# Performance work log

Measured on AMD Instinct MI355X. Metric: run time of the kernel, lower is better.

The kernel has to match this reference:

```python
import jax, jax.numpy as jnp
import numpy as np

EPS = 1e-6

def _phi(x):
    # elu(x) + 1 feature map
    return jax.nn.elu(x) + 1.0

def setup_inputs() -> dict:
    key = jax.random.key(0)
    kq, kk, kv = jax.random.split(key, 3)
    N, L, S, H, D, M = 8, 4096, 4096, 8, 64, 64
    queries = jax.random.normal(kq, (N, L, H, D), dtype=jnp.float32)
    keys = jax.random.normal(kk, (N, S, H, D), dtype=jnp.float32)
    values = jax.random.normal(kv, (N, S, H, M), dtype=jnp.float32)
    key_mask = jnp.ones((N, S), dtype=jnp.float32)  # key_lengths.float_matrix
    return {"queries": queries, "keys": keys, "values": values, "key_mask": key_mask}

def reference(queries, keys, values, key_mask):
    Q = _phi(queries)                                   # [N,L,H,D]
    K = _phi(keys) * key_mask[:, :, None, None]         # [N,S,H,D]
    KV = jnp.einsum('nshd,nshm->nhmd', K, values)       # [N,H,M,D]
    Z = 1.0 / (jnp.einsum('nlhd,nhd->nlh', Q, K.sum(axis=1)) + EPS)  # [N,L,H]
    V = jnp.einsum('nlhd,nhmd,nlh->nlhm', Q, KV, Z)     # [N,L,H,M]
    return V
```

## Files before the change

kernel.cpp:

```cpp
#include <hip/hip_runtime.h>


#define SLEN 4096
#define LLEN 4096
#define NHTOT 64
#define HD   512
#define NSPLIT 4
#define EPSF 1e-6f

__device__ __forceinline__ float phi(float x) {
    return x > 0.0f ? x + 1.0f : __expf(x);
}

__device__ __forceinline__ void fma4(float4& a, float s, const float4& b) {
    a.x = fmaf(s, b.x, a.x);
    a.y = fmaf(s, b.y, a.y);
    a.z = fmaf(s, b.z, a.z);
    a.w = fmaf(s, b.w, a.w);
}

__global__ __launch_bounds__(256)
void la_phase1(const float* __restrict__ Kg, const float* __restrict__ Vg,
               const float* __restrict__ maskg,
               float* __restrict__ KVp, float* __restrict__ Ksump) {
    __shared__ float kb[4][4096];
    __shared__ float vb[4][4096];
    __shared__ float ksb[16 * 64];

    const int tid  = threadIdx.x;
    const int w    = tid >> 6;
    const int lane = tid & 63;
    const int nh   = blockIdx.y;
    const int n    = nh >> 3;
    const int h    = nh & 7;
    const int sp   = blockIdx.x;

    const int sr4 = lane >> 4;
    const int c4  = (lane & 15) * 4;
    const int d0  = (lane & 7) * 8;
    const int m0  = (lane >> 3) * 8;

    float* kw = kb[w];
    float* vw = vb[w];

    const size_t base = (size_t)n * SLEN * HD + (size_t)h * 64;
    const float* mrow = maskg + (size_t)n * SLEN;

    float4 acc[8][2];
    #pragma unroll
    for (int i = 0; i < 8; ++i) {
        acc[i][0] = make_float4(0.f, 0.f, 0.f, 0.f);
        acc[i][1] = make_float4(0.f, 0.f, 0.f, 0.f);
    }
    float4 ksp = make_float4(0.f, 0.f, 0.f, 0.f);

    for (int t = 0; t < 4; ++t) {
        const int srow0 = sp * 1024 + t * 256 + w * 64;
        #pragma unroll
        for (int u = 0; u < 16; ++u) {
            const int row = sr4 + u * 4;
            const int s   = srow0 + row;
            const size_t g = base + (size_t)s * HD + c4;
            float4 kf = *(const float4*)(Kg + g);
            const float4 vf = *(const float4*)(Vg + g);
            const float mm = mrow[s];
            kf.x = phi(kf.x) * mm;
            kf.y = phi(kf.y) * mm;
            kf.z = phi(kf.z) * mm;
            kf.w = phi(kf.w) * mm;
            ksp.x += kf.x; ksp.y += kf.y; ksp.z += kf.z; ksp.w += kf.w;
            *(float4*)&kw[row * 64 + c4] = kf;
            *(float4*)&vw[row * 64 + c4] = vf;
        }
        #pragma unroll 4
        for (int s = 0; s < 64; ++s) {
            const float4 ka = *(const float4*)&kw[s * 64 + d0];
            const float4 kz = *(const float4*)&kw[s * 64 + d0 + 4];
            const float4 va = *(const float4*)&vw[s * 64 + m0];
            const float4 vz = *(const float4*)&vw[s * 64 + m0 + 4];
            fma4(acc[0][0], ka.x, va); fma4(acc[0][1], ka.x, vz);
            fma4(acc[1][0], ka.y, va); fma4(acc[1][1], ka.y, vz);
            fma4(acc[2][0], ka.z, va); fma4(acc[2][1], ka.z, vz);
            fma4(acc[3][0], ka.w, va); fma4(acc[3][1], ka.w, vz);
            fma4(acc[4][0], kz.x, va); fma4(acc[4][1], kz.x, vz);
            fma4(acc[5][0], kz.y, va); fma4(acc[5][1], kz.y, vz);
            fma4(acc[6][0], kz.z, va); fma4(acc[6][1], kz.z, vz);
            fma4(acc[7][0], kz.w, va); fma4(acc[7][1], kz.w, vz);
        }
    }

    *(float4*)&ksb[(w * 4 + sr4) * 64 + c4] = ksp;

    #pragma unroll
    for (int di = 0; di < 8; ++di) {
        *(float4*)&kw[(d0 + di) * 64 + m0]     = acc[di][0];
        *(float4*)&kw[(d0 + di) * 64 + m0 + 4] = acc[di][1];
    }
    __syncthreads();

    float* outp = KVp + ((size_t)sp * NHTOT + nh) * 4096;
    #pragma unroll
    for (int j = 0; j < 4; ++j) {
        const int f = (j * 256 + tid) * 4;
        float4 a  = *(const float4*)&kb[0][f];
        const float4 b1 = *(const float4*)&kb[1][f];
        const float4 b2 = *(const float4*)&kb[2][f];
        const float4 b3 = *(const float4*)&kb[3][f];
        a.x += b1.x + b2.x + b3.x;
        a.y += b1.y + b2.y + b3.y;
        a.z += b1.z + b2.z + b3.z;
        a.w += b1.w + b2.w + b3.w;
        *(float4*)&outp[f] = a;
    }
    if (tid < 64) {
        float ssum = 0.f;
        #pragma unroll
        for (int r = 0; r < 16; ++r) ssum += ksb[r * 64 + tid];
        Ksump[((size_t)sp * NHTOT + nh) * 64 + tid] = ssum;
    }
}

__global__ __launch_bounds__(256)
void la_reduce(const float* __restrict__ KVp, const float* __restrict__ Ksump,
               float* __restrict__ KVt, float* __restrict__ Ksum) {
    const int nh  = blockIdx.x;
    const int tid = threadIdx.x;
    #pragma unroll
    for (int j = 0; j < 4; ++j) {
        const int f = (j * 256 + tid) * 4;
        float4 a = make_float4(0.f, 0.f, 0.f, 0.f);
        #pragma unroll
        for (int s = 0; s < NSPLIT; ++s) {
            const float4 v = *(const float4*)&KVp[((size_t)s * NHTOT + nh) * 4096 + f];
            a.x += v.x; a.y += v.y; a.z += v.z; a.w += v.w;
        }
        *(float4*)&KVt[(size_t)nh * 4096 + f] = a;
    }
    if (tid < 64) {
        float a = 0.f;
        #pragma unroll
        for (int s = 0; s < NSPLIT; ++s)
            a += Ksump[((size_t)s * NHTOT + nh) * 64 + tid];
        Ksum[nh * 64 + tid] = a;
    }
}

__global__ __launch_bounds__(512)
void la_phase2(const float* __restrict__ Qg, const float* __restrict__ KVt,
               const float* __restrict__ Ksum, float* __restrict__ Og) {
    __shared__ float Qs[512 * 68];
    __shared__ float KVs[64 * 64];
    __shared__ float KSs[64];

    const int tid = threadIdx.x;
    const int nh  = blockIdx.y;
    const int n   = nh >> 3;
    const int h   = nh & 7;
    const int lbase = blockIdx.x * 512;

    #pragma unroll
    for (int j = 0; j < 2; ++j) {
        const int f = (j * 512 + tid) * 4;
        *(float4*)&KVs[f] = *(const float4*)&KVt[(size_t)nh * 4096 + f];
    }
    if (tid < 16) *(float4*)&KSs[tid * 4] = *(const float4*)&Ksum[nh * 64 + tid * 4];

    const int sr = tid >> 4;
    const int c4 = (tid & 15) * 4;
    #pragma unroll
    for (int u = 0; u < 16; ++u) {
        const int row = sr + u * 32;
        float4 q = *(const float4*)&Qg[((size_t)(n * LLEN + lbase + row) * 8 + h) * 64 + c4];
        q.x = phi(q.x); q.y = phi(q.y); q.z = phi(q.z); q.w = phi(q.w);
        *(float4*)&Qs[row * 68 + c4] = q;
    }
    __syncthreads();

    const int w    = tid >> 6;
    const int lane = tid & 63;
    const int ty   = lane >> 4;
    const int tx   = lane & 15;
    const int m0   = tx * 4;
    const int rb   = w * 64 + ty;

    float4 acc[16];
    float  den[16];
    #pragma unroll
    for (int i = 0; i < 16; ++i) {
        acc[i] = make_float4(0.f, 0.f, 0.f, 0.f);
        den[i] = 0.f;
    }

    for (int d4 = 0; d4 < 16; ++d4) {
        const float4 ks = *(const float4*)&KSs[d4 * 4];
        float4 q4[16];
        #pragma unroll
        for (int i = 0; i < 16; ++i)
            q4[i] = *(const float4*)&Qs[(rb + 4 * i) * 68 + d4 * 4];
        #pragma unroll
        for (int i = 0; i < 16; ++i) {
            den[i] = fmaf(q4[i].x, ks.x, den[i]);
            den[i] = fmaf(q4[i].y, ks.y, den[i]);
            den[i] = fmaf(q4[i].z, ks.z, den[i]);
            den[i] = fmaf(q4[i].w, ks.w, den[i]);
        }
        #pragma unroll
        for (int dk = 0; dk < 4; ++dk) {
            const float4 kv = *(const float4*)&KVs[(d4 * 4 + dk) * 64 + m0];
            #pragma unroll
            for (int i = 0; i < 16; ++i)
                fma4(acc[i], (&q4[i].x)[dk], kv);
        }
    }

    #pragma unroll
    for (int i = 0; i < 16; ++i) {
        const int l = lbase + rb + 4 * i;
        const float z = 1.0f / (den[i] + EPSF);
        float4 o = acc[i];
        o.x *= z; o.y *= z; o.z *= z; o.w *= z;
        *(float4*)&Og[((size_t)(n * LLEN + l) * 8 + h) * 64 + m0] = o;
    }
}

extern "C" void kernel_launch(void* const* d_in, const int* in_sizes, int n_in,
                              void* d_out, int out_size, void* d_ws, size_t ws_size,
                              hipStream_t stream) {
    const float* Q    = (const float*)d_in[0];
    const float* K    = (const float*)d_in[1];
    const float* V    = (const float*)d_in[2];
    const float* mask = (const float*)d_in[3];
    float* out = (float*)d_out;

    float* KVp   = (float*)d_ws;
    float* Ksump = KVp + (size_t)NSPLIT * NHTOT * 4096;
    float* KVt   = Ksump + (size_t)NSPLIT * NHTOT * 64;
    float* Ksum  = KVt + (size_t)NHTOT * 4096;

    dim3 g1(NSPLIT, NHTOT);
    la_phase1<<<g1, 256, 0, stream>>>(K, V, mask, KVp, Ksump);

    la_reduce<<<NHTOT, 256, 0, stream>>>(KVp, Ksump, KVt, Ksum);

    dim3 g2(LLEN / 512, NHTOT);
    la_phase2<<<g2, 512, 0, stream>>>(Q, KVt, Ksum, out);
}
```

Measured before the change: 274.4 us.

## Double split count, prefetch K/V in registers, shrink phase2 tiles with swizzled LDS

Phase1 doubles the S-split so there are more blocks, halves its shared memory and prefetches the next K/V chunk into registers while the current chunk is accumulated. The reduce kernel now spreads each head over four blocks. Phase2 uses 256-thread blocks with 8x8 per-thread tiles, an XOR-swizzled unpadded Q tile in LDS, and reads Ksum straight from global memory. The aim is more parallelism and occupancy plus hidden load latency, at the cost of more register pressure and a larger partial-sum reduction.

```diff
diff --git a/kernel.cpp b/kernel.cpp
--- a/kernel.cpp
+++ b/kernel.cpp
@@ -5,7 +5,7 @@
 #define LLEN 4096
 #define NHTOT 64
 #define HD   512
-#define NSPLIT 4
+#define NSPLIT 8
 #define EPSF 1e-6f
 
 __device__ __forceinline__ float phi(float x) {
@@ -19,12 +19,11 @@
     a.w = fmaf(s, b.w, a.w);
 }
 
-__global__ __launch_bounds__(256)
+__global__ __launch_bounds__(256, 2)
 void la_phase1(const float* __restrict__ Kg, const float* __restrict__ Vg,
                const float* __restrict__ maskg,
                float* __restrict__ KVp, float* __restrict__ Ksump) {
-    __shared__ float kb[4][4096];
-    __shared__ float vb[4][4096];
+    __shared__ float smem[4][4096];
     __shared__ float ksb[16 * 64];
 
     const int tid  = threadIdx.x;
@@ -40,11 +39,12 @@
     const int d0  = (lane & 7) * 8;
     const int m0  = (lane >> 3) * 8;
 
-    float* kw = kb[w];
-    float* vw = vb[w];
+    float* kw = smem[w];
+    float* vw = smem[w] + 2048;
 
     const size_t base = (size_t)n * SLEN * HD + (size_t)h * 64;
     const float* mrow = maskg + (size_t)n * SLEN;
+    const int wrow0 = sp * 512 + w * 128;
 
     float4 acc[8][2];
     #pragma unroll
@@ -54,26 +54,44 @@
     }
     float4 ksp = make_float4(0.f, 0.f, 0.f, 0.f);
 
+    float4 pk[8], pv[8];
+    float  pm[8];
+    #pragma unroll
+    for (int u = 0; u < 8; ++u) {
+        const int s = wrow0 + sr4 + u * 4;
+        const size_t g = base + (size_t)s * HD + c4;
+        pk[u] = *(const float4*)(Kg + g);
+        pv[u] = *(const float4*)(Vg + g);
+        pm[u] = mrow[s];
+    }
+
+    #pragma unroll
     for (int t = 0; t < 4; ++t) {
-        const int srow0 = sp * 1024 + t * 256 + w * 64;
-        #pragma unroll
-        for (int u = 0; u < 16; ++u) {
+        #pragma unroll
+        for (int u = 0; u < 8; ++u) {
             const int row = sr4 + u * 4;
-            const int s   = srow0 + row;
-            const size_t g = base + (size_t)s * HD + c4;
-            float4 kf = *(const float4*)(Kg + g);
-            const float4 vf = *(const float4*)(Vg + g);
-            const float mm = mrow[s];
+            float4 kf = pk[u];
+            const float mm = pm[u];
             kf.x = phi(kf.x) * mm;
             kf.y = phi(kf.y) * mm;
             kf.z = phi(kf.z) * mm;
             kf.w = phi(kf.w) * mm;
             ksp.x += kf.x; ksp.y += kf.y; ksp.z += kf.z; ksp.w += kf.w;
             *(float4*)&kw[row * 64 + c4] = kf;
-            *(float4*)&vw[row * 64 + c4] = vf;
+            *(float4*)&vw[row * 64 + c4] = pv[u];
+        }
+        if (t < 3) {
+            #pragma unroll
+            for (int u = 0; u < 8; ++u) {
+                const int s = wrow0 + (t + 1) * 32 + sr4 + u * 4;
+                const size_t g = base + (size_t)s * HD + c4;
+                pk[u] = *(const float4*)(Kg + g);
+                pv[u] = *(const float4*)(Vg + g);
+                pm[u] = mrow[s];
+            }
         }
         #pragma unroll 4
-        for (int s = 0; s < 64; ++s) {
+        for (int s = 0; s < 32; ++s) {
             const float4 ka = *(const float4*)&kw[s * 64 + d0];
             const float4 kz = *(const float4*)&kw[s * 64 + d0 + 4];
             const float4 va = *(const float4*)&vw[s * 64 + m0];
@@ -93,8 +111,8 @@
 
     #pragma unroll
     for (int di = 0; di < 8; ++di) {
-        *(float4*)&kw[(d0 + di) * 64 + m0]     = acc[di][0];
-        *(float4*)&kw[(d0 + di) * 64 + m0 + 4] = acc[di][1];
+        *(float4*)&smem[w][(d0 + di) * 64 + m0]     = acc[di][0];
+        *(float4*)&smem[w][(d0 + di) * 64 + m0 + 4] = acc[di][1];
     }
     __syncthreads();
 
@@ -102,10 +120,10 @@
     #pragma unroll
     for (int j = 0; j < 4; ++j) {
         const int f = (j * 256 + tid) * 4;
-        float4 a  = *(const float4*)&kb[0][f];
-        const float4 b1 = *(const float4*)&kb[1][f];
-        const float4 b2 = *(const float4*)&kb[2][f];
-        const float4 b3 = *(const float4*)&kb[3][f];
+        float4 a  = *(const float4*)&smem[0][f];
+        const float4 b1 = *(const float4*)&smem[1][f];
+        const float4 b2 = *(const float4*)&smem[2][f];
+        const float4 b3 = *(const float4*)&smem[3][f];
         a.x += b1.x + b2.x + b3.x;
         a.y += b1.y + b2.y + b3.y;
         a.z += b1.z + b2.z + b3.z;
@@ -123,82 +141,81 @@
 __global__ __launch_bounds__(256)
 void la_reduce(const float* __restrict__ KVp, const float* __restrict__ Ksump,
                float* __restrict__ KVt, float* __restrict__ Ksum) {
-    const int nh  = blockIdx.x;
+    const int nh  = blockIdx.x >> 2;
+    const int j   = blockIdx.x & 3;
     const int tid = threadIdx.x;
-    #pragma unroll
-    for (int j = 0; j < 4; ++j) {
-        const int f = (j * 256 + tid) * 4;
-        float4 a = make_float4(0.f, 0.f, 0.f, 0.f);
-        #pragma unroll
-        for (int s = 0; s < NSPLIT; ++s) {
-            const float4 v = *(const float4*)&KVp[((size_t)s * NHTOT + nh) * 4096 + f];
-            a.x += v.x; a.y += v.y; a.z += v.z; a.w += v.w;
-        }
-        *(float4*)&KVt[(size_t)nh * 4096 + f] = a;
-    }
-    if (tid < 64) {
-        float a = 0.f;
+    const int f = (j * 256 + tid) * 4;
+    float4 a = make_float4(0.f, 0.f, 0.f, 0.f);
+    #pragma unroll
+    for (int s = 0; s < NSPLIT; ++s) {
+        const float4 v = *(const float4*)&KVp[((size_t)s * NHTOT + nh) * 4096 + f];
+        a.x += v.x; a.y += v.y; a.z += v.z; a.w += v.w;
+    }
+    *(float4*)&KVt[(size_t)nh * 4096 + f] = a;
+    if (j == 0 && tid < 64) {
+        float b = 0.f;
         #pragma unroll
         for (int s = 0; s < NSPLIT; ++s)
-            a += Ksump[((size_t)s * NHTOT + nh) * 64 + tid];
-        Ksum[nh * 64 + tid] = a;
-    }
-}
-
-__global__ __launch_bounds__(512)
+            b += Ksump[((size_t)s * NHTOT + nh) * 64 + tid];
+        Ksum[nh * 64 + tid] = b;
+    }
+}
+
+__global__ __launch_bounds__(256, 2)
 void la_phase2(const float* __restrict__ Qg, const float* __restrict__ KVt,
                const float* __restrict__ Ksum, float* __restrict__ Og) {
-    __shared__ float Qs[512 * 68];
+    __shared__ float Qs[256 * 64];
     __shared__ float KVs[64 * 64];
-    __shared__ float KSs[64];
 
     const int tid = threadIdx.x;
     const int nh  = blockIdx.y;
     const int n   = nh >> 3;
     const int h   = nh & 7;
-    const int lbase = blockIdx.x * 512;
-
-    #pragma unroll
-    for (int j = 0; j < 2; ++j) {
-        const int f = (j * 512 + tid) * 4;
+    const int lbase = blockIdx.x * 256;
+
+    #pragma unroll
+    for (int j = 0; j < 4; ++j) {
+        const int f = (j * 256 + tid) * 4;
         *(float4*)&KVs[f] = *(const float4*)&KVt[(size_t)nh * 4096 + f];
     }
-    if (tid < 16) *(float4*)&KSs[tid * 4] = *(const float4*)&Ksum[nh * 64 + tid * 4];
 
     const int sr = tid >> 4;
-    const int c4 = (tid & 15) * 4;
+    const int cc = tid & 15;
     #pragma unroll
     for (int u = 0; u < 16; ++u) {
-        const int row = sr + u * 32;
-        float4 q = *(const float4*)&Qg[((size_t)(n * LLEN + lbase + row) * 8 + h) * 64 + c4];
+        const int row = u * 16 + sr;
+        float4 q = *(const float4*)&Qg[((size_t)(n * LLEN + lbase + row) * 8 + h) * 64 + cc * 4];
         q.x = phi(q.x); q.y = phi(q.y); q.z = phi(q.z); q.w = phi(q.w);
-        *(float4*)&Qs[row * 68 + c4] = q;
+        *(float4*)&Qs[row * 64 + (cc ^ (row & 7)) * 4] = q;
     }
     __syncthreads();
 
     const int w    = tid >> 6;
     const int lane = tid & 63;
-    const int ty   = lane >> 4;
-    const int tx   = lane & 15;
-    const int m0   = tx * 4;
+    const int ty   = lane >> 3;
+    const int tx   = lane & 7;
+    const int m0   = tx * 8;
     const int rb   = w * 64 + ty;
 
-    float4 acc[16];
-    float  den[16];
-    #pragma unroll
-    for (int i = 0; i < 16; ++i) {
-        acc[i] = make_float4(0.f, 0.f, 0.f, 0.f);
+    float4 acc[8][2];
+    float  den[8];
+    #pragma unroll
+    for (int i = 0; i < 8; ++i) {
+        acc[i][0] = make_float4(0.f, 0.f, 0.f, 0.f);
+        acc[i][1] = make_float4(0.f, 0.f, 0.f, 0.f);
         den[i] = 0.f;
     }
 
+    const float* ksrow = Ksum + nh * 64;
+
     for (int d4 = 0; d4 < 16; ++d4) {
-        const float4 ks = *(const float4*)&KSs[d4 * 4];
-        float4 q4[16];
-        #pragma unroll
-        for (int i = 0; i < 16; ++i)
-            q4[i] = *(const float4*)&Qs[(rb + 4 * i) * 68 + d4 * 4];
-        #pragma unroll
-        for (int i = 0; i < 16; ++i) {
+        const float4 ks = *(const float4*)&ksrow[d4 * 4];
+        float4 q4[8];
+        #pragma unroll
+        for (int i = 0; i < 8; ++i)
+            q4[i] = *(const float4*)&Qs[(rb + 8 * i) * 64 + ((d4 ^ ty) * 4)];
+        #pragma unroll
+        for (int i = 0; i < 8; ++i) {
             den[i] = fmaf(q4[i].x, ks.x, den[i]);
             den[i] = fmaf(q4[i].y, ks.y, den[i]);
             den[i] = fmaf(q4[i].z, ks.z, den[i]);
@@ -206,20 +223,27 @@
         }
         #pragma unroll
         for (int dk = 0; dk < 4; ++dk) {
-            const float4 kv = *(const float4*)&KVs[(d4 * 4 + dk) * 64 + m0];
+            const float4 kva = *(const float4*)&KVs[(d4 * 4 + dk) * 64 + m0];
+            const float4 kvz = *(const float4*)&KVs[(d4 * 4 + dk) * 64 + m0 + 4];
             #pragma unroll
-            for (int i = 0; i < 16; ++i)
-                fma4(acc[i], (&q4[i].x)[dk], kv);
-        }
-    }
-
-    #pragma unroll
-    for (int i = 0; i < 16; ++i) {
-        const int l = lbase + rb + 4 * i;
+            for (int i = 0; i < 8; ++i) {
+                const float qv = (&q4[i].x)[dk];
+                fma4(acc[i][0], qv, kva);
+                fma4(acc[i][1], qv, kvz);
+            }
+        }
+    }
+
+    #pragma unroll
+    for (int i = 0; i < 8; ++i) {
+        const int l = lbase + rb + 8 * i;
         const float z = 1.0f / (den[i] + EPSF);
-        float4 o = acc[i];
-        o.x *= z; o.y *= z; o.z *= z; o.w *= z;
-        *(float4*)&Og[((size_t)(n * LLEN + l) * 8 + h) * 64 + m0] = o;
+        float4 o0 = acc[i][0], o1 = acc[i][1];
+        o0.x *= z; o0.y *= z; o0.z *= z; o0.w *= z;
+        o1.x *= z; o1.y *= z; o1.z *= z; o1.w *= z;
+        float* op = &Og[((size_t)(n * LLEN + l) * 8 + h) * 64 + m0];
+        *(float4*)op       = o0;
+        *(float4*)(op + 4) = o1;
     }
 }
 
@@ -240,8 +264,8 @@
     dim3 g1(NSPLIT, NHTOT);
     la_phase1<<<g1, 256, 0, stream>>>(K, V, mask, KVp, Ksump);
 
-    la_reduce<<<NHTOT, 256, 0, stream>>>(KVp, Ksump, KVt, Ksum);
-
-    dim3 g2(LLEN / 512, NHTOT);
-    la_phase2<<<g2, 512, 0, stream>>>(Q, KVt, Ksum, out);
-}
+    la_reduce<<<256, 256, 0, stream>>>(KVp, Ksump, KVt, Ksum);
+
+    dim3 g2(LLEN / 256, NHTOT);
+    la_phase2<<<g2, 256, 0, stream>>>(Q, KVt, Ksum, out);
+}
```

Result: faster. 262.1 us (-4.5%).
